# Kernel optimization log

Hardware: AMD Instinct MI355X
Metric: run time of the kernel (lower is better)

## Reference

```python
import jax, jax.numpy as jnp
import numpy as np

B = 64
D = 4096          # width of every layer
# DAG: layer k consumes concat of prior layer outputs listed here (0 = input x)
CONNECTIONS = {1: [0], 2: [0, 1], 3: [1, 2], 4: [2, 3]}


def setup_inputs() -> dict:
    key = jax.random.key(0)
    keys = iter(jax.random.split(key, 32))
    inp = {"x": jax.random.normal(next(keys), (B, D), dtype=jnp.float32)}
    for k, v in CONNECTIONS.items():
        fan_in = D * len(v)
        bound = 1.0 / np.sqrt(fan_in)
        # kaiming_uniform_(a=sqrt(5)) -> U(-sqrt(6/((1+5)*fan_in)), +) = U(-1/sqrt(fan_in), +)
        inp[f"W{k}"] = jax.random.uniform(next(keys), (D, fan_in), jnp.float32, -bound, bound)
        inp[f"b{k}"] = jax.random.uniform(next(keys), (D,), jnp.float32, -bound, bound)
        # static binary mask (buffer in torch), stored as float like MaskedLinear expects
        inp[f"M{k}"] = (jax.random.uniform(next(keys), (D, fan_in)) < 0.5).astype(jnp.float32)
    return inp


def _dag_forward(x, Ws, bs, Ms):
    layer_output = [x]
    for k, v in CONNECTIONS.items():
        inputs = jnp.concatenate([layer_output[v_] for v_ in v], axis=1)  # [B, D*len(v)]
        # masked linear: y = inputs @ (W*M)^T + b, then ReLU
        y = jnp.einsum('bi,oi->bo', inputs, Ws[k] * Ms[k]) + bs[k]
        layer_output.append(jax.nn.relu(y))
    return layer_output[-1]


def reference(x, W1, b1, M1, W2, b2, M2, W3, b3, M3, W4, b4, M4):
    Ws = {1: W1, 2: W2, 3: W3, 4: W4}
    bs = {1: b1, 2: b2, 3: b3, 4: b4}
    Ms = {1: M1, 2: M2, 3: M3, 4: M4}
    return _dag_forward(x, Ws, bs, Ms)
```

## Files before the change

kernel.cpp:

```cpp
#include <hip/hip_runtime.h>
#include <hip/hip_bf16.h>
#include <stdint.h>


typedef __attribute__((ext_vector_type(8))) short  s8v;
typedef __attribute__((ext_vector_type(4))) float  f4v;
typedef __attribute__((ext_vector_type(2))) float  f2v;
typedef __attribute__((ext_vector_type(4))) unsigned short us4v;
typedef __attribute__((ext_vector_type(2))) unsigned short us2v;

#define LDA 16384
#define MFMA16 __builtin_amdgcn_mfma_f32_16x16x32_bf16

typedef __attribute__((address_space(3))) void       lds_void;
typedef const __attribute__((address_space(1))) void g_void;

__device__ __forceinline__ short f2bf(float f) {
  unsigned int u = __builtin_bit_cast(unsigned int, f);
  u += 0x7fffu + ((u >> 16) & 1u);
  return (short)(u >> 16);
}
__device__ __forceinline__ float bf2f(short s) {
  unsigned int u = ((unsigned int)(unsigned short)s) << 16;
  return __builtin_bit_cast(float, u);
}

__global__ void dag_splitx(const float* __restrict__ x,
                           ushort* __restrict__ xh, ushort* __restrict__ xl) {
  int idx = blockIdx.x * blockDim.x + threadIdx.x;
  int m = idx >> 10;
  int n = (idx & 1023) << 2;
  f4v v = *(const f4v*)(x + (size_t)m * 4096 + n);
  us4v h, l;
#pragma unroll
  for (int j = 0; j < 4; ++j) {
    short hh = f2bf(v[j]);
    h[j] = (unsigned short)hh;
    l[j] = (unsigned short)f2bf(v[j] - bf2f(hh));
  }
  *(us4v*)(xh + (size_t)m * LDA + n) = h;
  *(us4v*)(xl + (size_t)m * LDA + n) = l;
}

struct RA { s8v ah0, ah1, ah2, ah3, al0, al1, al2, al3; };

template <int NSUPER>
__global__ __launch_bounds__(256, 1) void dag_gemm_phaseA(
    const ushort* __restrict__ Ah,
    const ushort* __restrict__ Al,
    const float*  __restrict__ W,
    const float*  __restrict__ Mm,
    float*        __restrict__ partial,
    int K) {
  extern __shared__ float smem[];
  const int tid  = threadIdx.x;
  const int wave = tid >> 6, lane = tid & 63;
  const int l15  = lane & 15, blk = lane >> 4;
  const int n0   = blockIdx.x * 128 + wave * 32;
  const int klen = NSUPER * 64;
  const int kbeg = blockIdx.y * klen;

  float* base = smem + wave * 8192;
  float* WL0 = base;
  float* ML0 = base + 2048;
  float* WL1 = base + 4096;
  float* ML1 = base + 6144;

  const int srow = lane >> 4;
  const int sc   = lane & 15;

  const ushort* ap  = Ah + (size_t)l15 * LDA + kbeg + blk * 8;
  const ushort* alp = Al + (size_t)l15 * LDA + kbeg + blk * 8;

  f4v acc[4][2];
#pragma unroll
  for (int i = 0; i < 4; ++i) {
    acc[i][0] = (f4v){0.f, 0.f, 0.f, 0.f};
    acc[i][1] = (f4v){0.f, 0.f, 0.f, 0.f};
  }
  RA a0, a1;

  auto GLDS = [&](int s, float* WB, float* MB) {
#pragma unroll
    for (int j = 0; j < 8; ++j) {
      int row4 = 4 * j + srow;
      int gc   = sc ^ (row4 & 15);
      const float* ws = W  + (size_t)(n0 + row4) * K + kbeg + s * 64 + gc * 4;
      const float* ms = Mm + (size_t)(n0 + row4) * K + kbeg + s * 64 + gc * 4;
      __builtin_amdgcn_global_load_lds((g_void*)ws, (lds_void*)(WB + j * 256),
                                       16, 0, 0);
      __builtin_amdgcn_global_load_lds((g_void*)ms, (lds_void*)(MB + j * 256),
                                       16, 0, 0);
    }
  };
  auto LOADA = [&](RA& r, int ko) {
    r.ah0 = *(const s8v*)(ap  + ko);
    r.ah1 = *(const s8v*)(ap  + (size_t)16 * LDA + ko);
    r.ah2 = *(const s8v*)(ap  + (size_t)32 * LDA + ko);
    r.ah3 = *(const s8v*)(ap  + (size_t)48 * LDA + ko);
    r.al0 = *(const s8v*)(alp + ko);
    r.al1 = *(const s8v*)(alp + (size_t)16 * LDA + ko);
    r.al2 = *(const s8v*)(alp + (size_t)32 * LDA + ko);
    r.al3 = *(const s8v*)(alp + (size_t)48 * LDA + ko);
  };

  auto KSTEP = [&](int kstep, RA& ra, float* WL, float* ML) {
    const int cc = kstep * 8 + blk * 2;
    const int c0 = cc ^ l15, c1 = (cc + 1) ^ l15;
    const float* wr0 = WL + l15 * 64;
    const float* wr1 = WL + (l15 + 16) * 64;
    const float* mr0 = ML + l15 * 64;
    const float* mr1 = ML + (l15 + 16) * 64;
    f4v w0a = *(const f4v*)(wr0 + c0 * 4), w0b = *(const f4v*)(wr0 + c1 * 4);
    f4v w1a = *(const f4v*)(wr1 + c0 * 4), w1b = *(const f4v*)(wr1 + c1 * 4);
    f4v m0a = *(const f4v*)(mr0 + c0 * 4), m0b = *(const f4v*)(mr0 + c1 * 4);
    f4v m1a = *(const f4v*)(mr1 + c0 * 4), m1b = *(const f4v*)(mr1 + c1 * 4);

    s8v wh0, wl0, wh1, wl1;
#pragma unroll
    for (int j = 0; j < 4; ++j) {
      { float ww = w0a[j] * m0a[j]; short h = f2bf(ww);
        wh0[j]     = h; wl0[j]     = f2bf(ww - bf2f(h)); }
      { float ww = w0b[j] * m0b[j]; short h = f2bf(ww);
        wh0[j + 4] = h; wl0[j + 4] = f2bf(ww - bf2f(h)); }
      { float ww = w1a[j] * m1a[j]; short h = f2bf(ww);
        wh1[j]     = h; wl1[j]     = f2bf(ww - bf2f(h)); }
      { float ww = w1b[j] * m1b[j]; short h = f2bf(ww);
        wh1[j + 4] = h; wl1[j + 4] = f2bf(ww - bf2f(h)); }
    }
    acc[0][0] = MFMA16(ra.ah0, wh0, acc[0][0], 0, 0, 0);
    acc[0][0] = MFMA16(ra.al0, wh0, acc[0][0], 0, 0, 0);
    acc[0][0] = MFMA16(ra.ah0, wl0, acc[0][0], 0, 0, 0);
    acc[1][0] = MFMA16(ra.ah1, wh0, acc[1][0], 0, 0, 0);
    acc[1][0] = MFMA16(ra.al1, wh0, acc[1][0], 0, 0, 0);
    acc[1][0] = MFMA16(ra.ah1, wl0, acc[1][0], 0, 0, 0);
    acc[2][0] = MFMA16(ra.ah2, wh0, acc[2][0], 0, 0, 0);
    acc[2][0] = MFMA16(ra.al2, wh0, acc[2][0], 0, 0, 0);
    acc[2][0] = MFMA16(ra.ah2, wl0, acc[2][0], 0, 0, 0);
    acc[3][0] = MFMA16(ra.ah3, wh0, acc[3][0], 0, 0, 0);
    acc[3][0] = MFMA16(ra.al3, wh0, acc[3][0], 0, 0, 0);
    acc[3][0] = MFMA16(ra.ah3, wl0, acc[3][0], 0, 0, 0);
    acc[0][1] = MFMA16(ra.ah0, wh1, acc[0][1], 0, 0, 0);
    acc[0][1] = MFMA16(ra.al0, wh1, acc[0][1], 0, 0, 0);
    acc[0][1] = MFMA16(ra.ah0, wl1, acc[0][1], 0, 0, 0);
    acc[1][1] = MFMA16(ra.ah1, wh1, acc[1][1], 0, 0, 0);
    acc[1][1] = MFMA16(ra.al1, wh1, acc[1][1], 0, 0, 0);
    acc[1][1] = MFMA16(ra.ah1, wl1, acc[1][1], 0, 0, 0);
    acc[2][1] = MFMA16(ra.ah2, wh1, acc[2][1], 0, 0, 0);
    acc[2][1] = MFMA16(ra.al2, wh1, acc[2][1], 0, 0, 0);
    acc[2][1] = MFMA16(ra.ah2, wl1, acc[2][1], 0, 0, 0);
    acc[3][1] = MFMA16(ra.ah3, wh1, acc[3][1], 0, 0, 0);
    acc[3][1] = MFMA16(ra.al3, wh1, acc[3][1], 0, 0, 0);
    acc[3][1] = MFMA16(ra.ah3, wl1, acc[3][1], 0, 0, 0);
  };

  GLDS(0, WL0, ML0);
  LOADA(a0, 0);
  LOADA(a1, 32);
  asm volatile("s_waitcnt vmcnt(16)" ::: "memory");
  __builtin_amdgcn_sched_barrier(0);

#pragma unroll
  for (int s = 0; s < NSUPER; ++s) {
    float* curW = (s & 1) ? WL1 : WL0;
    float* curM = (s & 1) ? ML1 : ML0;
    float* nxtW = (s & 1) ? WL0 : WL1;
    float* nxtM = (s & 1) ? ML0 : ML1;
    if (s + 1 < NSUPER) GLDS(s + 1, nxtW, nxtM);
    KSTEP(0, a0, curW, curM);
    if (s + 1 < NSUPER) LOADA(a0, (s + 1) * 64);
    KSTEP(1, a1, curW, curM);
    if (s + 1 < NSUPER) LOADA(a1, (s + 1) * 64 + 32);
    if (s + 1 < NSUPER) {
      asm volatile("s_waitcnt vmcnt(16)" ::: "memory");
      __builtin_amdgcn_sched_barrier(0);
    }
  }

  float* pout = partial + (size_t)blockIdx.y * (64 * 4096);
#pragma unroll
  for (int mt = 0; mt < 4; ++mt)
#pragma unroll
    for (int nt = 0; nt < 2; ++nt) {
      int n = n0 + nt * 16 + l15;
#pragma unroll
      for (int rr = 0; rr < 4; ++rr) {
        int m = mt * 16 + blk * 4 + rr;
        pout[(size_t)m * 4096 + n] = acc[mt][nt][rr];
      }
    }
}

__global__ void dag_phaseB(const float* __restrict__ partial, int splitk,
                           const float* __restrict__ bias,
                           ushort* __restrict__ yh, ushort* __restrict__ yl,
                           float* __restrict__ yf) {
  int idx = blockIdx.x * blockDim.x + threadIdx.x;
  int m = idx >> 11;
  int n = (idx & 2047) << 1;
  const float* p = partial + (size_t)m * 4096 + n;
  float s0 = 0.f, s1 = 0.f;
#pragma unroll 4
  for (int sp = 0; sp < splitk; ++sp) {
    f2v v = *(const f2v*)(p + (size_t)sp * (64 * 4096));
    s0 += v[0]; s1 += v[1];
  }
  const f2v bv = *(const f2v*)(bias + n);
  s0 = fmaxf(s0 + bv[0], 0.f);
  s1 = fmaxf(s1 + bv[1], 0.f);
  if (yf) {
    *(f2v*)(yf + (size_t)m * 4096 + n) = (f2v){s0, s1};
  } else {
    us2v h, l;
    short h0 = f2bf(s0); h[0] = (unsigned short)h0;
    l[0] = (unsigned short)f2bf(s0 - bf2f(h0));
    short h1 = f2bf(s1); h[1] = (unsigned short)h1;
    l[1] = (unsigned short)f2bf(s1 - bf2f(h1));
    *(us2v*)(yh + (size_t)m * LDA + n) = h;
    *(us2v*)(yl + (size_t)m * LDA + n) = l;
  }
}

extern "C" void kernel_launch(void* const* d_in, const int* in_sizes, int n_in,
                              void* d_out, int out_size, void* d_ws, size_t ws_size,
                              hipStream_t stream) {
  (void)in_sizes; (void)n_in; (void)out_size;
  const float* x = (const float*)d_in[0];
  struct L { const float *W, *b, *M; int K, incol, outcol; };
  L Ls[4] = {
      {(const float*)d_in[1],  (const float*)d_in[2],  (const float*)d_in[3],  4096, 0,    4096},
      {(const float*)d_in[4],  (const float*)d_in[5],  (const float*)d_in[6],  8192, 0,    8192},
      {(const float*)d_in[7],  (const float*)d_in[8],  (const float*)d_in[9],  8192, 4096, 12288},
      {(const float*)d_in[10], (const float*)d_in[11], (const float*)d_in[12], 8192, 8192, 16384},
  };
  float* out = (float*)d_out;

  char* ws = (char*)d_ws;
  ushort* Ah = (ushort*)ws;
  ushort* Al = (ushort*)(ws + (size_t)64 * LDA * 2);
  float* partial = (float*)(ws + (size_t)2 * 64 * LDA * 2);
  int SPLITK = 8;
  while (SPLITK > 4 &&
         ws_size < (size_t)4 * 1024 * 1024 + (size_t)SPLITK * 1024 * 1024)
    SPLITK >>= 1;

  const int smem = 131072;
  hipFuncSetAttribute((const void*)dag_gemm_phaseA<8>,
                      hipFuncAttributeMaxDynamicSharedMemorySize, smem);
  hipFuncSetAttribute((const void*)dag_gemm_phaseA<16>,
                      hipFuncAttributeMaxDynamicSharedMemorySize, smem);
  hipFuncSetAttribute((const void*)dag_gemm_phaseA<32>,
                      hipFuncAttributeMaxDynamicSharedMemorySize, smem);

  dag_splitx<<<256, 256, 0, stream>>>(x, Ah, Al);

  for (int k = 0; k < 4; ++k) {
    dim3 grid(32, SPLITK);
    const ushort* Ahp = Ah + Ls[k].incol;
    const ushort* Alp = Al + Ls[k].incol;
    int nsuper = (Ls[k].K / SPLITK) / 64;
    switch (nsuper) {
      case 8:
        dag_gemm_phaseA<8><<<grid, 256, smem, stream>>>(
            Ahp, Alp, Ls[k].W, Ls[k].M, partial, Ls[k].K);
        break;
      case 16:
        dag_gemm_phaseA<16><<<grid, 256, smem, stream>>>(
            Ahp, Alp, Ls[k].W, Ls[k].M, partial, Ls[k].K);
        break;
      default:
        dag_gemm_phaseA<32><<<grid, 256, smem, stream>>>(
            Ahp, Alp, Ls[k].W, Ls[k].M, partial, Ls[k].K);
        break;
    }
    bool last = (k == 3);
    dag_phaseB<<<512, 256, 0, stream>>>(
        partial, SPLITK, Ls[k].b,
        last ? (ushort*)nullptr : Ah + Ls[k].outcol,
        last ? (ushort*)nullptr : Al + Ls[k].outcol,
        last ? out : (float*)nullptr);
  }
}
```

Measured before the change: 253.0 us.

## Deepen phase-A pipeline to four-stage ring of 32-wide K steps

Restructures the split-K GEMM main loop from a double-buffered pair of 64-wide K super-steps into a 4-slot ring of 32-wide K steps, each prefetched three steps ahead. W/M tiles go global-to-LDS and A fragments go to registers. Waits become graded vmcnt counts instead of one wait per super-step, with an XOR swizzle re-derived for 32-float rows. The aim is to keep more memory requests in flight and hide HBM latency in this bandwidth-bound masked GEMM, at the cost of four live A register sets and finer-grained waits.

Result: slower. 264.7 us (+4.6%).

```diff
diff --git a/kernel.cpp b/kernel.cpp
--- a/kernel.cpp
+++ b/kernel.cpp
@@ -44,7 +44,7 @@
 
 struct RA { s8v ah0, ah1, ah2, ah3, al0, al1, al2, al3; };
 
-template <int NSUPER>
+template <int NSTEPS>
 __global__ __launch_bounds__(256, 1) void dag_gemm_phaseA(
     const ushort* __restrict__ Ah,
     const ushort* __restrict__ Al,
@@ -57,17 +57,12 @@
   const int wave = tid >> 6, lane = tid & 63;
   const int l15  = lane & 15, blk = lane >> 4;
   const int n0   = blockIdx.x * 128 + wave * 32;
-  const int klen = NSUPER * 64;
-  const int kbeg = blockIdx.y * klen;
+  const int kbeg = blockIdx.y * (NSTEPS * 32);
 
   float* base = smem + wave * 8192;
-  float* WL0 = base;
-  float* ML0 = base + 2048;
-  float* WL1 = base + 4096;
-  float* ML1 = base + 6144;
-
-  const int srow = lane >> 4;
-  const int sc   = lane & 15;
+  const int srow8 = lane >> 3;
+  const int c8    = lane & 7;
+  const int gc    = c8 ^ srow8;
 
   const ushort* ap  = Ah + (size_t)l15 * LDA + kbeg + blk * 8;
   const ushort* alp = Al + (size_t)l15 * LDA + kbeg + blk * 8;
@@ -78,15 +73,19 @@
     acc[i][0] = (f4v){0.f, 0.f, 0.f, 0.f};
     acc[i][1] = (f4v){0.f, 0.f, 0.f, 0.f};
   }
-  RA a0, a1;
-
-  auto GLDS = [&](int s, float* WB, float* MB) {
-#pragma unroll
-    for (int j = 0; j < 8; ++j) {
-      int row4 = 4 * j + srow;
-      int gc   = sc ^ (row4 & 15);
-      const float* ws = W  + (size_t)(n0 + row4) * K + kbeg + s * 64 + gc * 4;
-      const float* ms = Mm + (size_t)(n0 + row4) * K + kbeg + s * 64 + gc * 4;
+  RA a0, a1, a2, a3;
+  auto AREF = [&](int i) -> RA& { return i == 0 ? a0 : i == 1 ? a1
+                                       : i == 2 ? a2 : a3; };
+
+  auto GLDS = [&](int t) {
+    float* WB = base + (t & 3) * 2048;
+    float* MB = WB + 1024;
+    const size_t kofs = (size_t)kbeg + t * 32 + gc * 4;
+#pragma unroll
+    for (int j = 0; j < 4; ++j) {
+      int row = j * 8 + srow8;
+      const float* ws = W  + (size_t)(n0 + row) * K + kofs;
+      const float* ms = Mm + (size_t)(n0 + row) * K + kofs;
       __builtin_amdgcn_global_load_lds((g_void*)ws, (lds_void*)(WB + j * 256),
                                        16, 0, 0);
       __builtin_amdgcn_global_load_lds((g_void*)ms, (lds_void*)(MB + j * 256),
@@ -104,13 +103,15 @@
     r.al3 = *(const s8v*)(alp + (size_t)48 * LDA + ko);
   };
 
-  auto KSTEP = [&](int kstep, RA& ra, float* WL, float* ML) {
-    const int cc = kstep * 8 + blk * 2;
-    const int c0 = cc ^ l15, c1 = (cc + 1) ^ l15;
-    const float* wr0 = WL + l15 * 64;
-    const float* wr1 = WL + (l15 + 16) * 64;
-    const float* mr0 = ML + l15 * 64;
-    const float* mr1 = ML + (l15 + 16) * 64;
+  auto KSTEP = [&](int t, RA& ra) {
+    float* WL = base + (t & 3) * 2048;
+    float* ML = WL + 1024;
+    const int x  = l15 & 7;
+    const int c0 = (2 * blk) ^ x, c1 = (2 * blk + 1) ^ x;
+    const float* wr0 = WL + l15 * 32;
+    const float* wr1 = WL + (l15 + 16) * 32;
+    const float* mr0 = ML + l15 * 32;
+    const float* mr1 = ML + (l15 + 16) * 32;
     f4v w0a = *(const f4v*)(wr0 + c0 * 4), w0b = *(const f4v*)(wr0 + c1 * 4);
     f4v w1a = *(const f4v*)(wr1 + c0 * 4), w1b = *(const f4v*)(wr1 + c1 * 4);
     f4v m0a = *(const f4v*)(mr0 + c0 * 4), m0b = *(const f4v*)(mr0 + c1 * 4);
@@ -154,27 +155,23 @@
     acc[3][1] = MFMA16(ra.ah3, wl1, acc[3][1], 0, 0, 0);
   };
 
-  GLDS(0, WL0, ML0);
-  LOADA(a0, 0);
-  LOADA(a1, 32);
-  asm volatile("s_waitcnt vmcnt(16)" ::: "memory");
-  __builtin_amdgcn_sched_barrier(0);
-
-#pragma unroll
-  for (int s = 0; s < NSUPER; ++s) {
-    float* curW = (s & 1) ? WL1 : WL0;
-    float* curM = (s & 1) ? ML1 : ML0;
-    float* nxtW = (s & 1) ? WL0 : WL1;
-    float* nxtM = (s & 1) ? ML0 : ML1;
-    if (s + 1 < NSUPER) GLDS(s + 1, nxtW, nxtM);
-    KSTEP(0, a0, curW, curM);
-    if (s + 1 < NSUPER) LOADA(a0, (s + 1) * 64);
-    KSTEP(1, a1, curW, curM);
-    if (s + 1 < NSUPER) LOADA(a1, (s + 1) * 64 + 32);
-    if (s + 1 < NSUPER) {
-      asm volatile("s_waitcnt vmcnt(16)" ::: "memory");
-      __builtin_amdgcn_sched_barrier(0);
-    }
+  GLDS(0); LOADA(a0, 0);
+  GLDS(1); LOADA(a1, 32);
+  GLDS(2); LOADA(a2, 64);
+
+#pragma unroll
+  for (int t = 0; t < NSTEPS; ++t) {
+    if (t + 3 < NSTEPS) {
+      GLDS(t + 3);
+      LOADA(AREF((t + 3) & 3), (t + 3) * 32);
+    }
+    const int rem = NSTEPS - 1 - t;
+    if (rem >= 3)      asm volatile("s_waitcnt vmcnt(48)" ::: "memory");
+    else if (rem == 2) asm volatile("s_waitcnt vmcnt(32)" ::: "memory");
+    else if (rem == 1) asm volatile("s_waitcnt vmcnt(16)" ::: "memory");
+    else               asm volatile("s_waitcnt vmcnt(0)"  ::: "memory");
+    __builtin_amdgcn_sched_barrier(0);
+    KSTEP(t, AREF(t & 3));
   }
 
   float* pout = partial + (size_t)blockIdx.y * (64 * 4096);
@@ -245,12 +242,12 @@
     SPLITK >>= 1;
 
   const int smem = 131072;
-  hipFuncSetAttribute((const void*)dag_gemm_phaseA<8>,
-                      hipFuncAttributeMaxDynamicSharedMemorySize, smem);
   hipFuncSetAttribute((const void*)dag_gemm_phaseA<16>,
                       hipFuncAttributeMaxDynamicSharedMemorySize, smem);
   hipFuncSetAttribute((const void*)dag_gemm_phaseA<32>,
                       hipFuncAttributeMaxDynamicSharedMemorySize, smem);
+  hipFuncSetAttribute((const void*)dag_gemm_phaseA<64>,
+                      hipFuncAttributeMaxDynamicSharedMemorySize, smem);
 
   dag_splitx<<<256, 256, 0, stream>>>(x, Ah, Al);
 
@@ -258,18 +255,18 @@
     dim3 grid(32, SPLITK);
     const ushort* Ahp = Ah + Ls[k].incol;
     const ushort* Alp = Al + Ls[k].incol;
-    int nsuper = (Ls[k].K / SPLITK) / 64;
-    switch (nsuper) {
-      case 8:
-        dag_gemm_phaseA<8><<<grid, 256, smem, stream>>>(
-            Ahp, Alp, Ls[k].W, Ls[k].M, partial, Ls[k].K);
-        break;
+    int nsteps = (Ls[k].K / SPLITK) / 32;
+    switch (nsteps) {
       case 16:
         dag_gemm_phaseA<16><<<grid, 256, smem, stream>>>(
             Ahp, Alp, Ls[k].W, Ls[k].M, partial, Ls[k].K);
         break;
+      case 32:
+        dag_gemm_phaseA<32><<<grid, 256, smem, stream>>>(
+            Ahp, Alp, Ls[k].W, Ls[k].M, partial, Ls[k].K);
+        break;
       default:
-        dag_gemm_phaseA<32><<<grid, 256, smem, stream>>>(
+        dag_gemm_phaseA<64><<<grid, 256, smem, stream>>>(
             Ahp, Alp, Ls[k].W, Ls[k].M, partial, Ls[k].K);
         break;
     }
```
